# Kernel optimization log

Measured on AMD Instinct MI355X. Metric: run time of the kernel, lower is better.

Reference implementation:

```python
import jax, jax.numpy as jnp
import numpy as np

N, D, H, DH, DFF, E = 4096, 512, 8, 64, 2048, 65536


def setup_inputs() -> dict:
    key = jax.random.key(0)
    ks = jax.random.split(key, 20)
    g = lambda k, s: jax.random.normal(k, s, dtype=jnp.float32) * 0.02
    inp = {
        'x': jax.random.normal(ks[0], (N, D), dtype=jnp.float32),
        'edge_index': jax.random.randint(ks[1], (2, E), 0, N),
        'edge_attr': jax.random.uniform(ks[2], (E,), dtype=jnp.float32),
        'Wg': g(ks[3], (D, D)), 'bg': jnp.zeros((D,), jnp.float32),
        'ln1_s': jnp.ones((D,), jnp.float32), 'ln1_b': jnp.zeros((D,), jnp.float32),
        'Wq': g(ks[4], (D, D)), 'bq': jnp.zeros((D,), jnp.float32),
        'Wk': g(ks[5], (D, D)), 'bk': jnp.zeros((D,), jnp.float32),
        'Wv': g(ks[6], (D, D)), 'bv': jnp.zeros((D,), jnp.float32),
        'Wo': g(ks[7], (D, D)), 'bo': jnp.zeros((D,), jnp.float32),
        'ln2_s': jnp.ones((D,), jnp.float32), 'ln2_b': jnp.zeros((D,), jnp.float32),
        'W1': g(ks[8], (D, DFF)), 'b1': jnp.zeros((DFF,), jnp.float32),
        'W2': g(ks[9], (DFF, D)), 'b2': jnp.zeros((D,), jnp.float32),
        'Wa': g(ks[10], (2 * D, D)), 'ba': jnp.zeros((D,), jnp.float32),
    }
    return inp


def _ln(x, s, b):
    m = x.mean(-1, keepdims=True)
    v = ((x - m) ** 2).mean(-1, keepdims=True)
    return (x - m) * jax.lax.rsqrt(v + 1e-5) * s + b


def _gcn(x, edge_index, ew, Wg, bg):
    # GCNConv: linear, add self-loops (weight 1), sym deg normalization, scatter-add
    xt = x @ Wg                                   # [N, D]
    src = jnp.concatenate([edge_index[0], jnp.arange(N)])
    dst = jnp.concatenate([edge_index[1], jnp.arange(N)])
    w = jnp.concatenate([ew, jnp.ones((N,), ew.dtype)])
    deg = jax.ops.segment_sum(w, dst, num_segments=N)
    dinv = jnp.where(deg > 0, jax.lax.rsqrt(jnp.maximum(deg, 1e-12)), 0.0)
    coef = dinv[src] * w * dinv[dst]              # [E+N]
    out = jax.ops.segment_sum(xt[src] * coef[:, None], dst, num_segments=N)
    return out + bg


def _tfm(x, p):
    # pre-LN vanilla transformer block over all N nodes as one sequence
    h = _ln(x, p['ln1_s'], p['ln1_b'])
    q = (h @ p['Wq'] + p['bq']).reshape(N, H, DH)
    k = (h @ p['Wk'] + p['bk']).reshape(N, H, DH)
    v = (h @ p['Wv'] + p['bv']).reshape(N, H, DH)
    scores = jnp.einsum('nhd,mhd->hnm', q, k) / np.sqrt(DH)
    a = jax.nn.softmax(scores, axis=-1)
    o = jnp.einsum('hnm,mhd->nhd', a, v).reshape(N, D)
    x = x + o @ p['Wo'] + p['bo']
    h2 = _ln(x, p['ln2_s'], p['ln2_b'])
    mlp = jax.nn.gelu(h2 @ p['W1'] + p['b1']) @ p['W2'] + p['b2']
    return x + mlp


def reference(x, edge_index, edge_attr, Wg, bg, ln1_s, ln1_b, Wq, bq, Wk, bk, Wv, bv,
              Wo, bo, ln2_s, ln2_b, W1, b1, W2, b2, Wa, ba):
    p = dict(ln1_s=ln1_s, ln1_b=ln1_b, Wq=Wq, bq=bq, Wk=Wk, bk=bk, Wv=Wv, bv=bv,
             Wo=Wo, bo=bo, ln2_s=ln2_s, ln2_b=ln2_b, W1=W1, b1=b1, W2=W2, b2=b2)
    mp = _gcn(x, edge_index, edge_attr, Wg, bg)
    tf = _tfm(x, p)
    return x + jnp.concatenate([mp, tf], axis=-1) @ Wa + ba
```

## Files before the change

### kernel.cpp

```cpp
#include <hip/hip_runtime.h>
#include <math.h>

#define N_NODES 4096
#define DMODEL  512
#define NHEAD   8
#define DHEAD   64
#define DFF     2048
#define NEDGE   65536
#define QKVLD   1536

typedef unsigned short u16;
typedef __bf16 bf16x8 __attribute__((ext_vector_type(8)));
typedef float  f32x4  __attribute__((ext_vector_type(4)));
typedef short  s16x4  __attribute__((ext_vector_type(4)));

#if defined(__has_builtin)
#if __has_builtin(__builtin_amdgcn_mfma_f32_16x16x16bf16_1k)
#define HAS_MFMA_1K 1
#endif
#endif

__device__ inline float fast_exp2(float x) {
    return __builtin_amdgcn_exp2f(x);
}

__device__ inline f32x4 mfma16(bf16x8 a, bf16x8 b, f32x4 c) {
    return __builtin_amdgcn_mfma_f32_16x16x32_bf16(a, b, c, 0, 0, 0);
}

#ifdef HAS_MFMA_1K
__device__ inline f32x4 mfma1k(s16x4 a, s16x4 b, f32x4 c) {
    return __builtin_amdgcn_mfma_f32_16x16x16bf16_1k(a, b, c, 0, 0, 0);
}
__device__ inline s16x4 pack_bf4(f32x4 p) {
    union { float f; unsigned u; } a0, a1, a2, a3;
    a0.f = p[0]; a1.f = p[1]; a2.f = p[2]; a3.f = p[3];
    unsigned lo = __builtin_amdgcn_perm(a1.u + 0x8000u, a0.u + 0x8000u, 0x07060302u);
    unsigned hi = __builtin_amdgcn_perm(a3.u + 0x8000u, a2.u + 0x8000u, 0x07060302u);
    union { unsigned u[2]; s16x4 v; } r;
    r.u[0] = lo; r.u[1] = hi;
    return r.v;
}
#endif

__device__ inline u16 f2bf(float f) {
    union { float f; unsigned u; } v; v.f = f;
    unsigned r = v.u + 0x7fff + ((v.u >> 16) & 1);
    return (u16)(r >> 16);
}

__device__ inline float bf2f(u16 v) {
    union { unsigned u; float f; } t; t.u = ((unsigned)v) << 16; return t.f;
}

__device__ inline float gelu_tanh(float x) {
    float x3 = x * x * x;
    float t = tanhf(0.7978845608028654f * (x + 0.044715f * x3));
    return 0.5f * x * (1.0f + t);
}

#define GBN 128
#define GBK 32
#define GP  40

template <int ACT, int OBF16>
__launch_bounds__(512)
__global__ void mfma_gemm64(const u16* __restrict__ A, const u16* __restrict__ Bt,
                            const float* __restrict__ bias, const float* __restrict__ res,
                            void* __restrict__ Cout, int M, int Nn, int K, float scale,
                            int ldC, int ldRes) {
    __shared__ u16 Asm[2][64 * GP];
    __shared__ u16 Bsm[2][128 * GP];

    const int tid = threadIdx.x;
    const int w = tid >> 6;
    const int lane = tid & 63;
    const int quad = lane >> 4;
    const int l15 = lane & 15;
    const int row0 = blockIdx.y * 64;
    const int col0 = blockIdx.x * GBN;
    const int rh = (w & 1) * 32;
    const int cg = (w >> 1) * 32;

    f32x4 acc[2][2];
#pragma unroll
    for (int i = 0; i < 2; ++i)
#pragma unroll
        for (int j = 0; j < 2; ++j) acc[i][j] = (f32x4){0.f, 0.f, 0.f, 0.f};

    const int brow = tid >> 2, bk = (tid & 3) * 8;
    const int arow = (tid & 255) >> 2, ak = (tid & 3) * 8;
    const bool doA = (tid < 256);

    {
        uint4 b0 = *(const uint4*)&Bt[(size_t)(col0 + brow) * K + bk];
        *(uint4*)&Bsm[0][brow * GP + bk] = b0;
        if (doA) {
            uint4 a0 = *(const uint4*)&A[(size_t)(row0 + arow) * K + ak];
            *(uint4*)&Asm[0][arow * GP + ak] = a0;
        }
    }
    __syncthreads();

    const int nT = K / GBK;
    for (int t = 0; t < nT; ++t) {
        const int buf = t & 1;
        uint4 an, bn;
        if (t + 1 < nT) {
            const int k0 = (t + 1) * GBK;
            bn = *(const uint4*)&Bt[(size_t)(col0 + brow) * K + k0 + bk];
            if (doA) an = *(const uint4*)&A[(size_t)(row0 + arow) * K + k0 + ak];
        }
        bf16x8 af[2], bf[2];
#pragma unroll
        for (int i = 0; i < 2; ++i)
            af[i] = *(const bf16x8*)&Asm[buf][(rh + i * 16 + l15) * GP + quad * 8];
#pragma unroll
        for (int j = 0; j < 2; ++j)
            bf[j] = *(const bf16x8*)&Bsm[buf][(cg + j * 16 + l15) * GP + quad * 8];
#pragma unroll
        for (int i = 0; i < 2; ++i)
#pragma unroll
            for (int j = 0; j < 2; ++j)
                acc[i][j] = mfma16(af[i], bf[j], acc[i][j]);
        if (t + 1 < nT) {
            *(uint4*)&Bsm[buf ^ 1][brow * GP + bk] = bn;
            if (doA) *(uint4*)&Asm[buf ^ 1][arow * GP + ak] = an;
            __syncthreads();
        }
    }

#pragma unroll
    for (int j = 0; j < 2; ++j) {
        const int col = col0 + cg + j * 16 + l15;
        const float bc = bias ? bias[col] : 0.f;
#pragma unroll
        for (int i = 0; i < 2; ++i) {
#pragma unroll
            for (int r = 0; r < 4; ++r) {
                const int row = row0 + rh + i * 16 + quad * 4 + r;
                float o = (acc[i][j][r] + bc) * scale;
                if (ACT == 1) o = gelu_tanh(o);
                if (res) o += res[(size_t)row * ldRes + col];
                if (OBF16)
                    ((u16*)Cout)[(size_t)row * ldC + col] = f2bf(o);
                else
                    ((float*)Cout)[(size_t)row * ldC + col] = o;
            }
        }
    }
}

__device__ inline uint4 reduce8_norm(const u16* b0, const u16* b1, const u16* b2,
                                     const u16* b3, size_t off, float linv) {
    const size_t OFF = (size_t)N_NODES * DMODEL;
    float s[8] = {0.f, 0.f, 0.f, 0.f, 0.f, 0.f, 0.f, 0.f};
    const u16* bs[4] = {b0, b1, b2, b3};
#pragma unroll
    for (int b = 0; b < 4; ++b)
#pragma unroll
        for (int k = 0; k < 2; ++k) {
            uint4 v = *(const uint4*)(bs[b] + k * OFF + off);
            unsigned uu[4] = {v.x, v.y, v.z, v.w};
#pragma unroll
            for (int t = 0; t < 4; ++t) {
                s[2 * t]     += bf2f((u16)(uu[t] & 0xffff));
                s[2 * t + 1] += bf2f((u16)(uu[t] >> 16));
            }
        }
    uint4 r;
    r.x = (unsigned)f2bf(s[0] * linv) | ((unsigned)f2bf(s[1] * linv) << 16);
    r.y = (unsigned)f2bf(s[2] * linv) | ((unsigned)f2bf(s[3] * linv) << 16);
    r.z = (unsigned)f2bf(s[4] * linv) | ((unsigned)f2bf(s[5] * linv) << 16);
    r.w = (unsigned)f2bf(s[6] * linv) | ((unsigned)f2bf(s[7] * linv) << 16);
    return r;
}

__launch_bounds__(512)
__global__ void wo_gemm(const u16* __restrict__ Ob0, const u16* __restrict__ Ob1,
                        const u16* __restrict__ Ob2, const u16* __restrict__ Ob3,
                        const float* __restrict__ lpart, const u16* __restrict__ Bt,
                        const float* __restrict__ bias, const float* __restrict__ res,
                        float* __restrict__ Cout) {
    __shared__ u16 Asm[2][64 * GP];
    __shared__ u16 Bsm[2][128 * GP];

    const int tid = threadIdx.x;
    const int w = tid >> 6;
    const int lane = tid & 63;
    const int quad = lane >> 4;
    const int l15 = lane & 15;
    const int row0 = blockIdx.y * 64;
    const int col0 = blockIdx.x * GBN;
    const int rh = (w & 1) * 32;
    const int cg = (w >> 1) * 32;
    const int K = DMODEL;

    f32x4 acc[2][2];
#pragma unroll
    for (int i = 0; i < 2; ++i)
#pragma unroll
        for (int j = 0; j < 2; ++j) acc[i][j] = (f32x4){0.f, 0.f, 0.f, 0.f};

    const int brow = tid >> 2, bk = (tid & 3) * 8;
    const int arow = (tid & 255) >> 2, ak = (tid & 3) * 8;
    const bool doA = (tid < 256);

    float linv[8];
    if (doA) {
        const float* lr = lpart + (size_t)(row0 + arow) * 64;
        float ls[8] = {0.f, 0.f, 0.f, 0.f, 0.f, 0.f, 0.f, 0.f};
#pragma unroll
        for (int v = 0; v < 16; ++v) {
            float4 q = *(const float4*)&lr[v * 4];
            ls[(v * 4 + 0) & 7] += q.x;
            ls[(v * 4 + 1) & 7] += q.y;
            ls[(v * 4 + 2) & 7] += q.z;
            ls[(v * 4 + 3) & 7] += q.w;
        }
#pragma unroll
        for (int hh = 0; hh < 8; ++hh) linv[hh] = 1.0f / ls[hh];
    }

    {
        uint4 b0 = *(const uint4*)&Bt[(size_t)(col0 + brow) * K + bk];
        *(uint4*)&Bsm[0][brow * GP + bk] = b0;
        if (doA) {
            uint4 a0 = reduce8_norm(Ob0, Ob1, Ob2, Ob3,
                                    (size_t)(row0 + arow) * DMODEL + ak, linv[0]);
            *(uint4*)&Asm[0][arow * GP + ak] = a0;
        }
    }
    __syncthreads();

#pragma unroll
    for (int t = 0; t < 16; ++t) {
        const int buf = t & 1;
        uint4 an, bn;
        if (t + 1 < 16) {
            const int k0 = (t + 1) * GBK;
            bn = *(const uint4*)&Bt[(size_t)(col0 + brow) * K + k0 + bk];
            if (doA)
                an = reduce8_norm(Ob0, Ob1, Ob2, Ob3,
                                  (size_t)(row0 + arow) * DMODEL + k0 + ak,
                                  linv[(t + 1) >> 1]);
        }
        bf16x8 af[2], bf[2];
#pragma unroll
        for (int i = 0; i < 2; ++i)
            af[i] = *(const bf16x8*)&Asm[buf][(rh + i * 16 + l15) * GP + quad * 8];
#pragma unroll
        for (int j = 0; j < 2; ++j)
            bf[j] = *(const bf16x8*)&Bsm[buf][(cg + j * 16 + l15) * GP + quad * 8];
#pragma unroll
        for (int i = 0; i < 2; ++i)
#pragma unroll
            for (int j = 0; j < 2; ++j)
                acc[i][j] = mfma16(af[i], bf[j], acc[i][j]);
        if (t + 1 < 16) {
            *(uint4*)&Bsm[buf ^ 1][brow * GP + bk] = bn;
            if (doA) *(uint4*)&Asm[buf ^ 1][arow * GP + ak] = an;
            __syncthreads();
        }
    }

#pragma unroll
    for (int j = 0; j < 2; ++j) {
        const int col = col0 + cg + j * 16 + l15;
        const float bc = bias[col];
#pragma unroll
        for (int i = 0; i < 2; ++i) {
#pragma unroll
            for (int r = 0; r < 4; ++r) {
                const int row = row0 + rh + i * 16 + quad * 4 + r;
                Cout[(size_t)row * DMODEL + col] =
                    acc[i][j][r] + bc + res[(size_t)row * DMODEL + col];
            }
        }
    }
}

#define QSCALE 0.1803368801111204f

__launch_bounds__(256)
__global__ void qkvg_gemm(const u16* __restrict__ xb, const u16* __restrict__ hb,
                          const u16* __restrict__ Wall,
                          const float* __restrict__ bq, const float* __restrict__ bk,
                          const float* __restrict__ bv,
                          u16* __restrict__ xtb, u16* __restrict__ qkvb,
                          u16* __restrict__ vtb) {
    __shared__ u16 Asm[2][64 * GP];
    __shared__ u16 Bsm[2][128 * GP];

    const int tid = threadIdx.x;
    const int w = tid >> 6;
    const int lane = tid & 63;
    const int quad = lane >> 4;
    const int l15 = lane & 15;
    const int row0 = blockIdx.y * 64;
    const int col0 = blockIdx.x * GBN;
    const int wn = w * 32;
    const int K = DMODEL;
    const u16* A = (col0 < 512) ? xb : hb;

    f32x4 acc[4][2];
#pragma unroll
    for (int i = 0; i < 4; ++i)
#pragma unroll
        for (int j = 0; j < 2; ++j) acc[i][j] = (f32x4){0.f, 0.f, 0.f, 0.f};

    const int c1 = tid, c2 = tid + 256;
    const int ar1 = c1 >> 2, ak1 = (c1 & 3) * 8;
    const int ar2 = c2 >> 2, ak2 = (c2 & 3) * 8;

    {
        uint4 a0 = *(const uint4*)&A   [(size_t)(row0 + ar1) * K + ak1];
        uint4 b0 = *(const uint4*)&Wall[(size_t)(col0 + ar1) * K + ak1];
        uint4 b1 = *(const uint4*)&Wall[(size_t)(col0 + ar2) * K + ak2];
        *(uint4*)&Asm[0][ar1 * GP + ak1] = a0;
        *(uint4*)&Bsm[0][ar1 * GP + ak1] = b0;
        *(uint4*)&Bsm[0][ar2 * GP + ak2] = b1;
    }
    __syncthreads();

    const int nT = K / GBK;
    for (int t = 0; t < nT; ++t) {
        const int buf = t & 1;
        uint4 an, bn0, bn1;
        if (t + 1 < nT) {
            const int k0 = (t + 1) * GBK;
            an  = *(const uint4*)&A   [(size_t)(row0 + ar1) * K + k0 + ak1];
            bn0 = *(const uint4*)&Wall[(size_t)(col0 + ar1) * K + k0 + ak1];
            bn1 = *(const uint4*)&Wall[(size_t)(col0 + ar2) * K + k0 + ak2];
        }
        bf16x8 af[4], bf[2];
#pragma unroll
        for (int i = 0; i < 4; ++i)
            af[i] = *(const bf16x8*)&Asm[buf][(i * 16 + l15) * GP + quad * 8];
#pragma unroll
        for (int j = 0; j < 2; ++j)
            bf[j] = *(const bf16x8*)&Bsm[buf][(wn + j * 16 + l15) * GP + quad * 8];
#pragma unroll
        for (int i = 0; i < 4; ++i)
#pragma unroll
            for (int j = 0; j < 2; ++j)
                acc[i][j] = mfma16(af[i], bf[j], acc[i][j]);
        if (t + 1 < nT) {
            *(uint4*)&Asm[buf ^ 1][ar1 * GP + ak1] = an;
            *(uint4*)&Bsm[buf ^ 1][ar1 * GP + ak1] = bn0;
            *(uint4*)&Bsm[buf ^ 1][ar2 * GP + ak2] = bn1;
            __syncthreads();
        }
    }

#pragma unroll
    for (int j = 0; j < 2; ++j) {
        const int col = col0 + wn + j * 16 + l15;
        if (col < 512) {
#pragma unroll
            for (int i = 0; i < 4; ++i)
#pragma unroll
                for (int r = 0; r < 4; ++r)
                    xtb[(size_t)(row0 + i * 16 + quad * 4 + r) * 512 + col] =
                        f2bf(acc[i][j][r]);
        } else if (col < 1536) {
            const float bc = (col < 1024) ? bq[col - 512] : bk[col - 1024];
            const float scale = (col < 1024) ? QSCALE : 1.0f;
#pragma unroll
            for (int i = 0; i < 4; ++i)
#pragma unroll
                for (int r = 0; r < 4; ++r)
                    qkvb[(size_t)(row0 + i * 16 + quad * 4 + r) * QKVLD + col - 512] =
                        f2bf((acc[i][j][r] + bc) * scale);
        } else {
            const int hd = col - 1536;
            const float bc = bv[hd];
#pragma unroll
            for (int i = 0; i < 4; ++i) {
                ushort4 pk;
                pk.x = f2bf(acc[i][j][0] + bc);
                pk.y = f2bf(acc[i][j][1] + bc);
                pk.z = f2bf(acc[i][j][2] + bc);
                pk.w = f2bf(acc[i][j][3] + bc);
                *(uint2*)&vtb[(size_t)hd * N_NODES + row0 + i * 16 + quad * 4] =
                    *(uint2*)&pk;
            }
        }
    }
}

__device__ inline float block_sum_256(float v, float* red4) {
#pragma unroll
    for (int o = 32; o > 0; o >>= 1) v += __shfl_down(v, o, 64);
    const int lane = threadIdx.x & 63;
    const int w = threadIdx.x >> 6;
    if (lane == 0) red4[w] = v;
    __syncthreads();
    return red4[0] + red4[1] + red4[2] + red4[3];
}

__launch_bounds__(256)
__global__ void prep_kernel(
    const float* __restrict__ Wg, const float* __restrict__ Wq,
    const float* __restrict__ Wk, const float* __restrict__ Wv,
    const float* __restrict__ Wo, const float* __restrict__ W1,
    const float* __restrict__ W2, const float* __restrict__ Wa,
    u16* __restrict__ Wgt, u16* __restrict__ Wqt, u16* __restrict__ Wkt,
    u16* __restrict__ Wvt, u16* __restrict__ Wot, u16* __restrict__ W1t,
    u16* __restrict__ W2t, u16* __restrict__ Wat,
    const float* __restrict__ x, u16* __restrict__ xb,
    const float* __restrict__ ln1s, const float* __restrict__ ln1b,
    u16* __restrict__ hb, float* __restrict__ deg, int* __restrict__ cnt) {
    __shared__ u16 t[32][34];
    __shared__ float redA[4];
    __shared__ float redB[4];
    const int id = blockIdx.x;

    if (id < 3840) {
        const float* W; u16* Wt; int K, Nn, bx, by;
        if (id < 1280) {
            const int m = id >> 8, tt = id & 255;
            bx = tt & 15; by = tt >> 4; K = 512; Nn = 512;
            W  = (m == 0) ? Wg  : (m == 1) ? Wq  : (m == 2) ? Wk  : (m == 3) ? Wv  : Wo;
            Wt = (m == 0) ? Wgt : (m == 1) ? Wqt : (m == 2) ? Wkt : (m == 3) ? Wvt : Wot;
        } else if (id < 2304) {
            const int tt = id - 1280; bx = tt & 63; by = tt >> 6;
            K = 512; Nn = 2048; W = W1; Wt = W1t;
        } else if (id < 3328) {
            const int tt = id - 2304; bx = tt & 15; by = tt >> 4;
            K = 2048; Nn = 512; W = W2; Wt = W2t;
        } else {
            const int tt = id - 3328; bx = tt & 15; by = tt >> 4;
            K = 1024; Nn = 512; W = Wa; Wt = Wat;
        }
        const int k0 = by * 32, n0 = bx * 32;
        const int r = threadIdx.x >> 3, c4 = (threadIdx.x & 7) * 4;
        float4 v = *(const float4*)&W[(size_t)(k0 + r) * Nn + n0 + c4];
        t[r][c4 + 0] = f2bf(v.x); t[r][c4 + 1] = f2bf(v.y);
        t[r][c4 + 2] = f2bf(v.z); t[r][c4 + 3] = f2bf(v.w);
        __syncthreads();
        u16 tmp[4];
#pragma unroll
        for (int i = 0; i < 4; ++i) tmp[i] = t[c4 + i][r];
        u16* op = Wt + (size_t)(n0 + r) * K + k0 + c4;
        *(uint2*)op = *(uint2*)tmp;
    } else if (id < 7936) {
        const int row = id - 3840;
        const int tid = threadIdx.x;
        const float* xr = x + (size_t)row * DMODEL;
        float v0 = xr[tid], v1 = xr[tid + 256];
        xb[(size_t)row * DMODEL + tid] = f2bf(v0);
        xb[(size_t)row * DMODEL + tid + 256] = f2bf(v1);
        float total = block_sum_256(v0 + v1, redA);
        float mean = total * (1.0f / DMODEL);
        float d0 = v0 - mean, d1 = v1 - mean;
        float sq = block_sum_256(d0 * d0 + d1 * d1, redB);
        float inv = rsqrtf(sq * (1.0f / DMODEL) + 1e-5f);
        hb[(size_t)row * DMODEL + tid] = f2bf(d0 * inv * ln1s[tid] + ln1b[tid]);
        hb[(size_t)row * DMODEL + tid + 256] =
            f2bf(d1 * inv * ln1s[tid + 256] + ln1b[tid + 256]);
    } else {
        int i = (id - 7936) * 256 + threadIdx.x;
        deg[i] = 1.0f;
        cnt[i] = 0;
    }
}

__launch_bounds__(256)
__global__ void ln_kernel(const float* __restrict__ X, const float* __restrict__ s,
                          const float* __restrict__ b, u16* __restrict__ Y) {
    __shared__ float redA[4];
    __shared__ float redB[4];
    const int row = blockIdx.x;
    const int tid = threadIdx.x;
    const float* xr = X + (size_t)row * DMODEL;
    float v0 = xr[tid], v1 = xr[tid + 256];
    float total = block_sum_256(v0 + v1, redA);
    float mean = total * (1.0f / DMODEL);
    float d0 = v0 - mean, d1 = v1 - mean;
    float sq = block_sum_256(d0 * d0 + d1 * d1, redB);
    float inv = rsqrtf(sq * (1.0f / DMODEL) + 1e-5f);
    Y[(size_t)row * DMODEL + tid] = f2bf(d0 * inv * s[tid] + b[tid]);
    Y[(size_t)row * DMODEL + tid + 256] = f2bf(d1 * inv * s[tid + 256] + b[tid + 256]);
}

__global__ void gcn_count_kernel(const int* __restrict__ ei, const float* __restrict__ ew,
                                 float* __restrict__ deg, int* __restrict__ cnt) {
    int e = blockIdx.x * 256 + threadIdx.x;
    int d = ei[NEDGE + e];
    atomicAdd(&cnt[d], 1);
    atomicAdd(&deg[d], ew[e]);
}

__launch_bounds__(256)
__global__ void gcn_prefix_kernel(const int* __restrict__ cnt, int* __restrict__ off,
                                  int* __restrict__ cur, const float* __restrict__ deg,
                                  float* __restrict__ dinv) {
    __shared__ int part[256];
    const int tid = threadIdx.x;
    int local[16];
    int s = 0;
#pragma unroll
    for (int i = 0; i < 16; ++i) { local[i] = s; s += cnt[tid * 16 + i]; }
    part[tid] = s;
#pragma unroll
    for (int i = 0; i < 16; ++i) {
        const int n = tid * 16 + i;
        float d = deg[n];
        dinv[n] = (d > 0.f) ? rsqrtf(fmaxf(d, 1e-12f)) : 0.f;
    }
    __syncthreads();
    if (tid == 0) {
        int run = 0;
        for (int j = 0; j < 256; ++j) { int t = part[j]; part[j] = run; run += t; }
        off[N_NODES] = run;
    }
    __syncthreads();
    int p = part[tid];
#pragma unroll
    for (int i = 0; i < 16; ++i) {
        off[tid * 16 + i] = p + local[i];
        cur[tid * 16 + i] = p + local[i];
    }
}

__global__ void gcn_fill_kernel(const int* __restrict__ ei, const float* __restrict__ ew,
                                int* __restrict__ cur, int* __restrict__ esrc,
                                float* __restrict__ eww) {
    int e = blockIdx.x * 256 + threadIdx.x;
    int s = ei[e], d = ei[NEDGE + e];
    int pos = atomicAdd(&cur[d], 1);
    esrc[pos] = s;
    eww[pos] = ew[e];
}

__launch_bounds__(256)
__global__ void gcn_gather_kernel(const u16* __restrict__ xtb, const int* __restrict__ off,
                                  const int* __restrict__ esrc, const float* __restrict__ eww,
                                  const float* __restrict__ dinv, const float* __restrict__ bg,
                                  u16* __restrict__ catb) {
    const int d = blockIdx.x;
    const int b0 = off[d], b1 = off[d + 1];
    const float did = dinv[d];
    const int c = threadIdx.x * 2;
    float a0 = 0.f, a1 = 0.f;
    for (int j = b0; j < b1; ++j) {
        const int s = esrc[j];
        const float coef = dinv[s] * eww[j] * did;
        const unsigned pv = *(const unsigned*)&xtb[(size_t)s * DMODEL + c];
        a0 += coef * bf2f((u16)(pv & 0xffff));
        a1 += coef * bf2f((u16)(pv >> 16));
    }
    {
        const unsigned pv = *(const unsigned*)&xtb[(size_t)d * DMODEL + c];
        const float sl = did * did;
        a0 += sl * bf2f((u16)(pv & 0xffff));
        a1 += sl * bf2f((u16)(pv >> 16));
    }
    const unsigned pk = (unsigned)f2bf(a0 + bg[c]) | ((unsigned)f2bf(a1 + bg[c + 1]) << 16);
    *(unsigned*)&catb[(size_t)d * 1024 + c] = pk;
}

#define TK 64
#define AP 72
#define NSPLIT 8
#define KSPAN (N_NODES / NSPLIT)

__launch_bounds__(256)
__global__ void attn_kernel(const u16* __restrict__ Qkv, const u16* __restrict__ Vtb,
                            u16* __restrict__ Ob0, u16* __restrict__ Ob1,
                            u16* __restrict__ Ob2, u16* __restrict__ Ob3,
                            float* __restrict__ lpart) {
    __shared__ u16 Ks[64 * AP];
    __shared__ u16 Vs[64 * AP];
#ifndef HAS_MFMA_1K
    __shared__ u16 Ps[4][2][16 * AP];
#endif

    const int h = blockIdx.x;
    const int q0 = blockIdx.y * 128;
    const int sp = blockIdx.z;
    u16* bases0 = (sp < 2) ? Ob0 : (sp < 4) ? Ob1 : (sp < 6) ? Ob2 : Ob3;
    u16* __restrict__ Opx = bases0 + (size_t)(sp & 1) * N_NODES * DMODEL;
    const int kbase = sp * KSPAN;

    const int tid = threadIdx.x;
    const int w = tid >> 6;
    const int lane = tid & 63;
    const int quad = lane >> 4;
    const int l15 = lane & 15;

    const u16* qp = Qkv + (size_t)(q0 + w * 32 + l15) * QKVLD + h * DHEAD + quad * 8;
    bf16x8 qf[2][2];
    qf[0][0] = *(const bf16x8*)qp;
    qf[0][1] = *(const bf16x8*)(qp + 32);
    qf[1][0] = *(const bf16x8*)(qp + 16 * QKVLD);
    qf[1][1] = *(const bf16x8*)(qp + 16 * QKVLD + 32);

    f32x4 Oa[2][4];
#pragma unroll
    for (int a = 0; a < 2; ++a)
#pragma unroll
        for (int g = 0; g < 4; ++g) Oa[a][g] = (f32x4){0.f, 0.f, 0.f, 0.f};
    float ls[2] = {0.f, 0.f};

    const int srow = (tid & 127) >> 1;
    const int scol = (tid & 1) * 32;

    for (int kt = kbase; kt < kbase + KSPAN; kt += TK) {
        if (tid < 128) {
            const uint4* kg = (const uint4*)(Qkv + (size_t)(kt + srow) * QKVLD + 512 + h * DHEAD + scol);
            uint4* kd = (uint4*)&Ks[srow * AP + scol];
            kd[0] = kg[0]; kd[1] = kg[1]; kd[2] = kg[2]; kd[3] = kg[3];
        } else {
            const uint4* vg = (const uint4*)(Vtb + ((size_t)h * DHEAD + srow) * N_NODES + kt + scol);
            uint4* vd = (uint4*)&Vs[srow * AP + scol];
            vd[0] = vg[0]; vd[1] = vg[1]; vd[2] = vg[2]; vd[3] = vg[3];
        }
        __syncthreads();

        f32x4 St[2][4];
#pragma unroll
        for (int f = 0; f < 4; ++f) {
            const u16* kr = &Ks[(f * 16 + l15) * AP + quad * 8];
            bf16x8 k0 = *(const bf16x8*)kr;
            bf16x8 k1 = *(const bf16x8*)(kr + 32);
#pragma unroll
            for (int a = 0; a < 2; ++a) {
                f32x4 z = (f32x4){0.f, 0.f, 0.f, 0.f};
                z = mfma16(k0, qf[a][0], z);
                St[a][f] = mfma16(k1, qf[a][1], z);
            }
        }

#ifdef HAS_MFMA_1K
        s16x4 pk[2][4];
#pragma unroll
        for (int a = 0; a < 2; ++a)
#pragma unroll
            for (int f = 0; f < 4; ++f) {
                f32x4 p;
                p[0] = fast_exp2(St[a][f][0]);
                p[1] = fast_exp2(St[a][f][1]);
                p[2] = fast_exp2(St[a][f][2]);
                p[3] = fast_exp2(St[a][f][3]);
                ls[a] += (p[0] + p[1]) + (p[2] + p[3]);
                pk[a][f] = pack_bf4(p);
            }
#pragma unroll
        for (int f = 0; f < 4; ++f)
#pragma unroll
            for (int g = 0; g < 4; ++g) {
                const s16x4 vv = *(const s16x4*)&Vs[(g * 16 + l15) * AP + f * 16 + quad * 4];
                Oa[0][g] = mfma1k(pk[0][f], vv, Oa[0][g]);
                Oa[1][g] = mfma1k(pk[1][f], vv, Oa[1][g]);
            }
#else
        bf16x8 pa[2][2];
#pragma unroll
        for (int a = 0; a < 2; ++a) {
            u16* pw = Ps[w][a];
#pragma unroll
            for (int f = 0; f < 4; ++f) {
                float p0 = fast_exp2(St[a][f][0]);
                float p1 = fast_exp2(St[a][f][1]);
                float p2 = fast_exp2(St[a][f][2]);
                float p3 = fast_exp2(St[a][f][3]);
                ls[a] += (p0 + p1) + (p2 + p3);
                ushort4 pkk;
                pkk.x = f2bf(p0); pkk.y = f2bf(p1); pkk.z = f2bf(p2); pkk.w = f2bf(p3);
                *(uint2*)&pw[l15 * AP + f * 16 + quad * 4] = *(uint2*)&pkk;
            }
            const u16* pr = &pw[l15 * AP + quad * 8];
            pa[a][0] = *(const bf16x8*)pr;
            pa[a][1] = *(const bf16x8*)(pr + 32);
        }
#pragma unroll
        for (int g = 0; g < 4; ++g) {
            const u16* vr = &Vs[(g * 16 + l15) * AP + quad * 8];
            bf16x8 v0 = *(const bf16x8*)vr;
            bf16x8 v1 = *(const bf16x8*)(vr + 32);
#pragma unroll
            for (int a = 0; a < 2; ++a) {
                Oa[a][g] = mfma16(pa[a][0], v0, Oa[a][g]);
                Oa[a][g] = mfma16(pa[a][1], v1, Oa[a][g]);
            }
        }
#endif
        __syncthreads();
    }

#pragma unroll
    for (int a = 0; a < 2; ++a) {
        float s = ls[a];
        s += __shfl_xor(s, 16, 64);
        s += __shfl_xor(s, 32, 64);
        const int rowbase = q0 + w * 32 + a * 16;
        if (quad == 0)
            lpart[(size_t)(rowbase + l15) * 64 + sp * 8 + h] = s;
#pragma unroll
        for (int r = 0; r < 4; ++r) {
            u16* op = Opx + (size_t)(rowbase + quad * 4 + r) * DMODEL + h * DHEAD + l15;
#pragma unroll
            for (int g = 0; g < 4; ++g) op[g * 16] = f2bf(Oa[a][g][r]);
        }
    }
}

static void mgemm64(hipStream_t st, const u16* A, const u16* Bt, const float* bias,
                    const float* res, void* C, int M, int Nn, int K, float scale,
                    int act, int obf16, int ldC, int ldRes) {
    dim3 g(Nn / GBN, M / 64), b(512);
    if (act)
        hipLaunchKernelGGL((mfma_gemm64<1, 1>), g, b, 0, st, A, Bt, bias, res, C, M, Nn, K, scale, ldC, ldRes);
    else if (obf16)
        hipLaunchKernelGGL((mfma_gemm64<0, 1>), g, b, 0, st, A, Bt, bias, res, C, M, Nn, K, scale, ldC, ldRes);
    else
        hipLaunchKernelGGL((mfma_gemm64<0, 0>), g, b, 0, st, A, Bt, bias, res, C, M, Nn, K, scale, ldC, ldRes);
}

extern "C" void kernel_launch(void* const* d_in, const int* in_sizes, int n_in,
                              void* d_out, int out_size, void* d_ws, size_t ws_size,
                              hipStream_t stream) {
    const float* x    = (const float*)d_in[0];
    const int*   ei   = (const int*)d_in[1];
    const float* ew   = (const float*)d_in[2];
    const float* Wg   = (const float*)d_in[3];
    const float* bg   = (const float*)d_in[4];
    const float* ln1s = (const float*)d_in[5];
    const float* ln1b = (const float*)d_in[6];
    const float* Wq   = (const float*)d_in[7];
    const float* bq   = (const float*)d_in[8];
    const float* Wk   = (const float*)d_in[9];
    const float* bk   = (const float*)d_in[10];
    const float* Wv   = (const float*)d_in[11];
    const float* bv   = (const float*)d_in[12];
    const float* Wo   = (const float*)d_in[13];
    const float* bo   = (const float*)d_in[14];
    const float* ln2s = (const float*)d_in[15];
    const float* ln2b = (const float*)d_in[16];
    const float* W1   = (const float*)d_in[17];
    const float* b1   = (const float*)d_in[18];
    const float* W2   = (const float*)d_in[19];
    const float* b2   = (const float*)d_in[20];
    const float* Wa   = (const float*)d_in[21];
    const float* ba   = (const float*)d_in[22];
    float* out = (float*)d_out;
    float* ws  = (float*)d_ws;

    const size_t SLOT = (size_t)N_NODES * DMODEL;

    u16* xtb = (u16*)ws;
    u16* Ob0 = (u16*)ws;
    float* lpart = ws + SLOT;
    int*   esrc  = (int*)(ws + SLOT + 327680);
    float* eww   = (float*)(esrc + NEDGE);
    int*   off   = (int*)(eww + NEDGE);
    int*   cur   = off + 4100;
    int*   cnt   = cur + 4096;
    u16* Ob1 = (u16*)(ws + 2 * SLOT);
    u16* hb  = (u16*)(ws + 3 * SLOT);
    u16* h2b = hb + SLOT;
    u16*   qkvb = (u16*)(ws + 4 * SLOT);
    float* x1   = ws + 4 * SLOT;
    u16*   vtb  = (u16*)(ws + 5 * SLOT) + SLOT;
    u16* Ob2  = (u16*)(ws + 6 * SLOT);
    u16* Ob3  = (u16*)(ws + 7 * SLOT);
    u16* midb = (u16*)(ws + 6 * SLOT);
    u16* catb = (u16*)(ws + 8 * SLOT);
    u16* xb   = catb;
    u16* Wgt = (u16*)(ws + 9 * SLOT);
    u16* Wqt = Wgt + 262144;
    u16* Wkt = Wqt + 262144;
    u16* Wvt = Wkt + 262144;
    u16* Wot = Wvt + 262144;
    u16* W1t = Wot + 262144;
    u16* W2t = W1t + 1048576;
    u16* Wat = W2t + 1048576;
    float* deg  = (float*)(Wat + 524288);
    float* dinv = deg + N_NODES;

    hipLaunchKernelGGL(prep_kernel, dim3(7952), dim3(256), 0, stream,
                       Wg, Wq, Wk, Wv, Wo, W1, W2, Wa,
                       Wgt, Wqt, Wkt, Wvt, Wot, W1t, W2t, Wat,
                       x, xb, ln1s, ln1b, hb, deg, cnt);

    hipLaunchKernelGGL(qkvg_gemm, dim3(16, 64), dim3(256), 0, stream,
                       xb, hb, Wgt, bq, bk, bv, xtb, qkvb, vtb);

    hipLaunchKernelGGL(gcn_count_kernel, dim3(NEDGE / 256), dim3(256), 0, stream, ei, ew, deg, cnt);
    hipLaunchKernelGGL(gcn_prefix_kernel, dim3(1), dim3(256), 0, stream, cnt, off, cur, deg, dinv);
    hipLaunchKernelGGL(gcn_fill_kernel, dim3(NEDGE / 256), dim3(256), 0, stream, ei, ew, cur, esrc, eww);
    hipLaunchKernelGGL(gcn_gather_kernel, dim3(N_NODES), dim3(256), 0, stream,
                       xtb, off, esrc, eww, dinv, bg, catb);

    hipLaunchKernelGGL(attn_kernel, dim3(NHEAD, N_NODES / 128, NSPLIT), dim3(256), 0, stream,
                       qkvb, vtb, Ob0, Ob1, Ob2, Ob3, lpart);

    hipLaunchKernelGGL(wo_gemm, dim3(4, 64), dim3(512), 0, stream,
                       Ob0, Ob1, Ob2, Ob3, lpart, Wot, bo, x, x1);

    hipLaunchKernelGGL(ln_kernel, dim3(N_NODES), dim3(256), 0, stream, x1, ln2s, ln2b, h2b);
    mgemm64(stream, h2b, W1t, b1, nullptr, midb, N_NODES, DFF, DMODEL, 1.0f, 1, 1, DFF, DFF);
    mgemm64(stream, midb, W2t, b2, x1, catb + 512, N_NODES, DMODEL, DFF, 1.0f, 0, 1, 1024, DMODEL);

    mgemm64(stream, catb, Wat, ba, x, out, N_NODES, DMODEL, 2 * DMODEL, 1.0f, 0, 0, DMODEL, DMODEL);
}
```

Before: 339.5 us.

## Double-buffer K/V tiles in attention with register prefetch and MFMA priority

```diff
diff --git a/kernel.cpp b/kernel.cpp
--- a/kernel.cpp
+++ b/kernel.cpp
@@ -571,8 +571,8 @@
                             u16* __restrict__ Ob0, u16* __restrict__ Ob1,
                             u16* __restrict__ Ob2, u16* __restrict__ Ob3,
                             float* __restrict__ lpart) {
-    __shared__ u16 Ks[64 * AP];
-    __shared__ u16 Vs[64 * AP];
+    __shared__ u16 Ks[2][64 * AP];
+    __shared__ u16 Vs[2][64 * AP];
 #ifndef HAS_MFMA_1K
     __shared__ u16 Ps[4][2][16 * AP];
 #endif
@@ -606,23 +606,42 @@
 
     const int srow = (tid & 127) >> 1;
     const int scol = (tid & 1) * 32;
-
-    for (int kt = kbase; kt < kbase + KSPAN; kt += TK) {
-        if (tid < 128) {
-            const uint4* kg = (const uint4*)(Qkv + (size_t)(kt + srow) * QKVLD + 512 + h * DHEAD + scol);
-            uint4* kd = (uint4*)&Ks[srow * AP + scol];
+    const bool isK = (tid < 128);
+
+    {
+        if (isK) {
+            const uint4* kg = (const uint4*)(Qkv + (size_t)(kbase + srow) * QKVLD + 512 + h * DHEAD + scol);
+            uint4* kd = (uint4*)&Ks[0][srow * AP + scol];
             kd[0] = kg[0]; kd[1] = kg[1]; kd[2] = kg[2]; kd[3] = kg[3];
         } else {
-            const uint4* vg = (const uint4*)(Vtb + ((size_t)h * DHEAD + srow) * N_NODES + kt + scol);
-            uint4* vd = (uint4*)&Vs[srow * AP + scol];
+            const uint4* vg = (const uint4*)(Vtb + ((size_t)h * DHEAD + srow) * N_NODES + kbase + scol);
+            uint4* vd = (uint4*)&Vs[0][srow * AP + scol];
             vd[0] = vg[0]; vd[1] = vg[1]; vd[2] = vg[2]; vd[3] = vg[3];
         }
-        __syncthreads();
+    }
+    __syncthreads();
+
+    const int NT = KSPAN / TK;
+    for (int t = 0; t < NT; ++t) {
+        const int buf = t & 1;
+        const bool more = (t + 1 < NT);
+        uint4 s0, s1, s2, s3;
+        if (more) {
+            const int kn = kbase + (t + 1) * TK;
+            if (isK) {
+                const uint4* kg = (const uint4*)(Qkv + (size_t)(kn + srow) * QKVLD + 512 + h * DHEAD + scol);
+                s0 = kg[0]; s1 = kg[1]; s2 = kg[2]; s3 = kg[3];
+            } else {
+                const uint4* vg = (const uint4*)(Vtb + ((size_t)h * DHEAD + srow) * N_NODES + kn + scol);
+                s0 = vg[0]; s1 = vg[1]; s2 = vg[2]; s3 = vg[3];
+            }
+        }
 
         f32x4 St[2][4];
+        __builtin_amdgcn_s_setprio(1);
 #pragma unroll
         for (int f = 0; f < 4; ++f) {
-            const u16* kr = &Ks[(f * 16 + l15) * AP + quad * 8];
+            const u16* kr = &Ks[buf][(f * 16 + l15) * AP + quad * 8];
             bf16x8 k0 = *(const bf16x8*)kr;
             bf16x8 k1 = *(const bf16x8*)(kr + 32);
 #pragma unroll
@@ -632,6 +651,7 @@
                 St[a][f] = mfma16(k1, qf[a][1], z);
             }
         }
+        __builtin_amdgcn_s_setprio(0);
 
 #ifdef HAS_MFMA_1K
         s16x4 pk[2][4];
@@ -647,14 +667,16 @@
                 ls[a] += (p[0] + p[1]) + (p[2] + p[3]);
                 pk[a][f] = pack_bf4(p);
             }
+        __builtin_amdgcn_s_setprio(1);
 #pragma unroll
         for (int f = 0; f < 4; ++f)
 #pragma unroll
             for (int g = 0; g < 4; ++g) {
-                const s16x4 vv = *(const s16x4*)&Vs[(g * 16 + l15) * AP + f * 16 + quad * 4];
+                const s16x4 vv = *(const s16x4*)&Vs[buf][(g * 16 + l15) * AP + f * 16 + quad * 4];
                 Oa[0][g] = mfma1k(pk[0][f], vv, Oa[0][g]);
                 Oa[1][g] = mfma1k(pk[1][f], vv, Oa[1][g]);
             }
+        __builtin_amdgcn_s_setprio(0);
 #else
         bf16x8 pa[2][2];
 #pragma unroll
@@ -675,9 +697,10 @@
             pa[a][0] = *(const bf16x8*)pr;
             pa[a][1] = *(const bf16x8*)(pr + 32);
         }
+        __builtin_amdgcn_s_setprio(1);
 #pragma unroll
         for (int g = 0; g < 4; ++g) {
-            const u16* vr = &Vs[(g * 16 + l15) * AP + quad * 8];
+            const u16* vr = &Vs[buf][(g * 16 + l15) * AP + quad * 8];
             bf16x8 v0 = *(const bf16x8*)vr;
             bf16x8 v1 = *(const bf16x8*)(vr + 32);
 #pragma unroll
@@ -686,8 +709,19 @@
                 Oa[a][g] = mfma16(pa[a][1], v1, Oa[a][g]);
             }
         }
+        __builtin_amdgcn_s_setprio(0);
 #endif
-        __syncthreads();
+
+        if (more) {
+            if (isK) {
+                uint4* kd = (uint4*)&Ks[buf ^ 1][srow * AP + scol];
+                kd[0] = s0; kd[1] = s1; kd[2] = s2; kd[3] = s3;
+            } else {
+                uint4* vd = (uint4*)&Vs[buf ^ 1][srow * AP + scol];
+                vd[0] = s0; vd[1] = s1; vd[2] = s2; vd[3] = s3;
+            }
+            __syncthreads();
+        }
     }
 
 #pragma unroll
```

New measurement: 331.4 us. 1.02x faster.
